# Optimization experiments

Measured on AMD Instinct MI355X. Metric: run time of the kernel, lower is better.

## Reference

```python
import jax, jax.numpy as jnp
import numpy as np

DT = 3600.0  # Euler step size (seconds)
N = 2_097_152  # number of timesteps = len(t)


def _get_AB(params):
    """Build the 3x3 A and 3x5 B RC-network matrices from the 7 parameters."""
    Cai, Cwe, Cwi, Re, Ri, Rw, Rg = (params[i] for i in range(7))
    z = jnp.zeros((), params.dtype)
    A = jnp.stack([
        jnp.stack([-1.0 / Cai * (1.0 / Rg + 1.0 / Ri), z, 1.0 / (Cai * Ri)]),
        jnp.stack([z, -1.0 / Cwe * (1.0 / Re + 1.0 / Rw), 1.0 / (Cwe * Rw)]),
        jnp.stack([1.0 / (Cwi * Ri), 1.0 / (Cwi * Rw), -1.0 / Cwi * (1.0 / Rw + 1.0 / Ri)]),
    ])  # [3,3]
    B = jnp.stack([
        jnp.stack([1.0 / (Cai * Rg), 1.0 / Cai, 1.0 / Cai, z, z]),
        jnp.stack([1.0 / (Cwe * Re), z, z, 1.0 / Cwe, z]),
        jnp.stack([z, z, z, z, 1.0 / Cwi]),
    ])  # [3,5]
    return A, B


def setup_inputs() -> dict:
    key = jax.random.key(0)
    d = jax.random.normal(key, (N, 5), dtype=jnp.float32)  # disturbance inputs per step
    params = jnp.array([100000.0, 30000.0, 300000.0, 10.0, 1.0, 10.0, 10.0], dtype=jnp.float32)
    x0 = jnp.array([20.0, 30.0, 26.0], dtype=jnp.float32)  # initial state temps
    return {"params": params, "x0": x0, "d": d}


def reference(params, x0, d):
    # One explicit-Euler step per timestep:
    #   x_{i+1} = x_i + dt*(A x_i + B d_i) = M x_i + c_i,  M = I + dt*A, c_i = dt*B d_i
    A, B = _get_AB(params)
    M = jnp.eye(3, dtype=params.dtype) + DT * A  # [3,3]
    c = DT * (d[:-1] @ B.T)  # [N-1,3]; last row of d is unused (loop runs len(t)-1 steps)

    def step(x, ci):
        xn = M @ x + ci
        return xn, xn

    _, xs = jax.lax.scan(step, x0, c)  # xs: [N-1,3]
    return jnp.concatenate([x0[None, :], xs], axis=0)  # [N,3] == x_all
```

## Files before the change

kernel.cpp:

```cpp
#include <hip/hip_runtime.h>


static constexpr long STEPS = 2097151;
static constexpr int  SEG   = 8;
static constexpr int  TPB   = 256;
static constexpr int  NBLK  = 1024;
static constexpr long NSEGT = (long)NBLK*TPB;

struct Coef {
    float m00,m02,m11,m12,m20,m21,m22;
    float b00,b01,b10,b13,b24;
};

__device__ __forceinline__ Coef derive(const float* __restrict__ p){
    Coef o;
    const float dt = 3600.0f;
    float Cai=p[0],Cwe=p[1],Cwi=p[2],Re=p[3],Ri=p[4],Rw=p[5],Rg=p[6];
    o.m00 = 1.0f + dt * (-1.0f/Cai*(1.0f/Rg + 1.0f/Ri));
    o.m02 = dt * (1.0f/(Cai*Ri));
    o.m11 = 1.0f + dt * (-1.0f/Cwe*(1.0f/Re + 1.0f/Rw));
    o.m12 = dt * (1.0f/(Cwe*Rw));
    o.m20 = dt * (1.0f/(Cwi*Ri));
    o.m21 = dt * (1.0f/(Cwi*Rw));
    o.m22 = 1.0f + dt * (-1.0f/Cwi*(1.0f/Rw + 1.0f/Ri));
    o.b00 = dt * (1.0f/(Cai*Rg));
    o.b01 = dt * (1.0f/Cai);
    o.b10 = dt * (1.0f/(Cwe*Re));
    o.b13 = dt * (1.0f/Cwe);
    o.b24 = dt * (1.0f/Cwi);
    return o;
}

__device__ __forceinline__ void step(const Coef& C, float& s0, float& s1, float& s2,
                                     float d0, float d1, float d2, float d3, float d4){
    float c0 = fmaf(C.b00, d0, C.b01*(d1+d2));
    float c1 = fmaf(C.b10, d0, C.b13*d3);
    float c2 = C.b24*d4;
    float n0 = fmaf(C.m00, s0, fmaf(C.m02, s2, c0));
    float n1 = fmaf(C.m11, s1, fmaf(C.m12, s2, c1));
    float n2 = fmaf(C.m20, s0, fmaf(C.m21, s1, fmaf(C.m22, s2, c2)));
    s0=n0; s1=n1; s2=n2;
}

__device__ __forceinline__ void mm3(const double* X, const double* Y, double* Z){
    #pragma unroll
    for (int r=0;r<3;++r)
        #pragma unroll
        for (int c=0;c<3;++c)
            Z[r*3+c] = X[r*3+0]*Y[0*3+c] + X[r*3+1]*Y[1*3+c] + X[r*3+2]*Y[2*3+c];
}
__device__ __forceinline__ void msq(double* X){ double T[9]; mm3(X,X,T);
    #pragma unroll
    for (int i=0;i<9;++i) X[i]=T[i]; }

__device__ __forceinline__ void computeM(const float* __restrict__ p, double* Md){
    double Cai=p[0],Cwe=p[1],Cwi=p[2],Re=p[3],Ri=p[4],Rw=p[5],Rg=p[6];
    const double dt = 3600.0;
    Md[0]=1.0 - dt*((1.0/Rg + 1.0/Ri)/Cai); Md[1]=0.0;                              Md[2]=dt/(Cai*Ri);
    Md[3]=0.0;                              Md[4]=1.0 - dt*((1.0/Re + 1.0/Rw)/Cwe); Md[5]=dt/(Cwe*Rw);
    Md[6]=dt/(Cwi*Ri);                      Md[7]=dt/(Cwi*Rw);                      Md[8]=1.0 - dt*((1.0/Rw + 1.0/Ri)/Cwi);
}

__device__ __forceinline__ void seg_sum(const float* __restrict__ d, long i0, const Coef& C,
                                        float& s0, float& s1, float& s2){
    const float4* dp = (const float4*)(d + i0*5);
    s0=0.f; s1=0.f; s2=0.f;
    #pragma unroll
    for (int g=0; g<2; ++g){
        float4 q0=dp[g*5+0], q1=dp[g*5+1], q2=dp[g*5+2], q3=dp[g*5+3], q4=dp[g*5+4];
        step(C,s0,s1,s2, q0.x,q0.y,q0.z,q0.w,q1.x);
        step(C,s0,s1,s2, q1.y,q1.z,q1.w,q2.x,q2.y);
        step(C,s0,s1,s2, q2.z,q2.w,q3.x,q3.y,q3.z);
        step(C,s0,s1,s2, q3.w,q4.x,q4.y,q4.z,q4.w);
    }
}

__global__ __launch_bounds__(256) void k_tot(const float* __restrict__ d,
                                             const float* __restrict__ p,
                                             float* __restrict__ blkTot){
    int t = threadIdx.x, b = blockIdx.x;
    long k = (long)b*TPB + t;
    Coef C = derive(p);
    float s0,s1,s2;
    seg_sum(d, k*SEG, C, s0,s1,s2);

    __shared__ float a[TPB*3];
    a[t*3+0]=s0; a[t*3+1]=s1; a[t*3+2]=s2;
    double Qd[9]; computeM(p, Qd);
    msq(Qd); msq(Qd); msq(Qd);
    __syncthreads();
    for (int off=1; off<TPB; off<<=1){
        float Qf[9];
        #pragma unroll
        for (int i=0;i<9;++i) Qf[i]=(float)Qd[i];
        if ((t & (2*off-1))==0){
            float l0=a[t*3+0], l1=a[t*3+1], l2=a[t*3+2];
            float r0=a[(t+off)*3+0], r1=a[(t+off)*3+1], r2=a[(t+off)*3+2];
            a[t*3+0] = r0 + Qf[0]*l0+Qf[1]*l1+Qf[2]*l2;
            a[t*3+1] = r1 + Qf[3]*l0+Qf[4]*l1+Qf[5]*l2;
            a[t*3+2] = r2 + Qf[6]*l0+Qf[7]*l1+Qf[8]*l2;
        }
        msq(Qd);
        __syncthreads();
    }
    if (t==0){ blkTot[b*3+0]=a[0]; blkTot[b*3+1]=a[1]; blkTot[b*3+2]=a[2]; }
}

__global__ __launch_bounds__(256) void k_scan(const float* __restrict__ d,
                                              const float* __restrict__ p,
                                              const float* __restrict__ blkTot,
                                              const float* __restrict__ x0,
                                              float* __restrict__ out){
    __shared__ float Tl[NBLK*3];
    __shared__ float Wl[TPB*3];
    __shared__ float Sl[TPB*3];
    __shared__ float powA[8][9];
    __shared__ float powB[8][9];
    __shared__ float Rm[9];

    int t = threadIdx.x, b = blockIdx.x;
    long k = (long)b*TPB + t;
    long i0 = k*SEG;
    Coef C = derive(p);

    for (int i=t; i<NBLK*3; i+=TPB) Tl[i] = blkTot[i];

    if (t==0){
        double Qd[9]; computeM(p, Qd);
        msq(Qd); msq(Qd); msq(Qd);
        for (int l=0;l<8;++l){
            #pragma unroll
            for (int i=0;i<9;++i) powA[l][i]=(float)Qd[i];
            msq(Qd);
        }
        #pragma unroll
        for (int i=0;i<9;++i) Rm[i]=(float)Qd[i];
        msq(Qd); msq(Qd);
        for (int l=0;l<8;++l){
            #pragma unroll
            for (int i=0;i<9;++i) powB[l][i]=(float)Qd[i];
            msq(Qd);
        }
    }
    __syncthreads();

    float x00=x0[0], x01=x0[1], x02=x0[2];
    if (t==0){
        Tl[0] += Rm[0]*x00+Rm[1]*x01+Rm[2]*x02;
        Tl[1] += Rm[3]*x00+Rm[4]*x01+Rm[5]*x02;
        Tl[2] += Rm[6]*x00+Rm[7]*x01+Rm[8]*x02;
    }
    __syncthreads();

    float w0=Tl[(4*t)*3+0], w1=Tl[(4*t)*3+1], w2=Tl[(4*t)*3+2];
    #pragma unroll
    for (int j=1;j<4;++j){
        float n0 = Tl[(4*t+j)*3+0] + Rm[0]*w0+Rm[1]*w1+Rm[2]*w2;
        float n1 = Tl[(4*t+j)*3+1] + Rm[3]*w0+Rm[4]*w1+Rm[5]*w2;
        float n2 = Tl[(4*t+j)*3+2] + Rm[6]*w0+Rm[7]*w1+Rm[8]*w2;
        w0=n0; w1=n1; w2=n2;
    }
    Wl[t*3+0]=w0; Wl[t*3+1]=w1; Wl[t*3+2]=w2;
    __syncthreads();
    for (int l=0;l<8;++l){
        int off = 1<<l;
        float y0=0.f,y1=0.f,y2=0.f;
        if (t>=off){ y0=Wl[(t-off)*3+0]; y1=Wl[(t-off)*3+1]; y2=Wl[(t-off)*3+2]; }
        __syncthreads();
        if (t>=off){
            w0 += powB[l][0]*y0+powB[l][1]*y1+powB[l][2]*y2;
            w1 += powB[l][3]*y0+powB[l][4]*y1+powB[l][5]*y2;
            w2 += powB[l][6]*y0+powB[l][7]*y1+powB[l][8]*y2;
            Wl[t*3+0]=w0; Wl[t*3+1]=w1; Wl[t*3+2]=w2;
        }
        __syncthreads();
    }

    float c0,c1,c2;
    if (b==0){ c0=x00; c1=x01; c2=x02; }
    else {
        int e = b-1, q = e>>2;
        float P0=0.f,P1=0.f,P2=0.f;
        if (q>0){ P0=Wl[(q-1)*3+0]; P1=Wl[(q-1)*3+1]; P2=Wl[(q-1)*3+2]; }
        for (int j=4*q; j<=e; ++j){
            float n0 = Tl[j*3+0] + Rm[0]*P0+Rm[1]*P1+Rm[2]*P2;
            float n1 = Tl[j*3+1] + Rm[3]*P0+Rm[4]*P1+Rm[5]*P2;
            float n2 = Tl[j*3+2] + Rm[6]*P0+Rm[7]*P1+Rm[8]*P2;
            P0=n0; P1=n1; P2=n2;
        }
        c0=P0; c1=P1; c2=P2;
    }

    float s0,s1,s2;
    seg_sum(d, i0, C, s0,s1,s2);
    float v0=s0, v1=s1, v2=s2;
    if (t==0){
        v0 += powA[0][0]*c0+powA[0][1]*c1+powA[0][2]*c2;
        v1 += powA[0][3]*c0+powA[0][4]*c1+powA[0][5]*c2;
        v2 += powA[0][6]*c0+powA[0][7]*c1+powA[0][8]*c2;
    }
    Sl[t*3+0]=v0; Sl[t*3+1]=v1; Sl[t*3+2]=v2;
    __syncthreads();
    for (int l=0;l<8;++l){
        int off = 1<<l;
        float y0=0.f,y1=0.f,y2=0.f;
        if (t>=off){ y0=Sl[(t-off)*3+0]; y1=Sl[(t-off)*3+1]; y2=Sl[(t-off)*3+2]; }
        __syncthreads();
        if (t>=off){
            v0 += powA[l][0]*y0+powA[l][1]*y1+powA[l][2]*y2;
            v1 += powA[l][3]*y0+powA[l][4]*y1+powA[l][5]*y2;
            v2 += powA[l][6]*y0+powA[l][7]*y1+powA[l][8]*y2;
            Sl[t*3+0]=v0; Sl[t*3+1]=v1; Sl[t*3+2]=v2;
        }
        __syncthreads();
    }

    float g0,g1,g2;
    if (t==0){ g0=c0; g1=c1; g2=c2; }
    else     { g0=Sl[(t-1)*3+0]; g1=Sl[(t-1)*3+1]; g2=Sl[(t-1)*3+2]; }

    if (k==0){ out[0]=x00; out[1]=x01; out[2]=x02; }
    const float4* dp = (const float4*)(d + i0*5);
    float* op = out + (i0+1)*3;
    bool full = (k != NSEGT-1);
    #pragma unroll
    for (int g=0; g<2; ++g){
        float4 q0=dp[g*5+0], q1=dp[g*5+1], q2=dp[g*5+2], q3=dp[g*5+3], q4=dp[g*5+4];
        step(C,g0,g1,g2, q0.x,q0.y,q0.z,q0.w,q1.x);
        op[(g*4+0)*3+0]=g0; op[(g*4+0)*3+1]=g1; op[(g*4+0)*3+2]=g2;
        step(C,g0,g1,g2, q1.y,q1.z,q1.w,q2.x,q2.y);
        op[(g*4+1)*3+0]=g0; op[(g*4+1)*3+1]=g1; op[(g*4+1)*3+2]=g2;
        step(C,g0,g1,g2, q2.z,q2.w,q3.x,q3.y,q3.z);
        op[(g*4+2)*3+0]=g0; op[(g*4+2)*3+1]=g1; op[(g*4+2)*3+2]=g2;
        step(C,g0,g1,g2, q3.w,q4.x,q4.y,q4.z,q4.w);
        if (g==1 && !full) break;
        op[(g*4+3)*3+0]=g0; op[(g*4+3)*3+1]=g1; op[(g*4+3)*3+2]=g2;
    }
}

extern "C" void kernel_launch(void* const* d_in, const int* in_sizes, int n_in,
                              void* d_out, int out_size, void* d_ws, size_t ws_size,
                              hipStream_t stream) {
    const float* params = (const float*)d_in[0];
    const float* x0     = (const float*)d_in[1];
    const float* d      = (const float*)d_in[2];
    float* out    = (float*)d_out;
    float* blkTot = (float*)d_ws;

    k_tot <<<NBLK, TPB, 0, stream>>>(d, params, blkTot);
    k_scan<<<NBLK, TPB, 0, stream>>>(d, params, blkTot, x0, out);
}
```

Baseline: 45.84 us.

## Stage chunk inputs through LDS with coalesced loads and stores, restructure block-carry scan

Both kernels now load each block's 2048-row chunk of d into shared memory with fully coalesced float4 reads, replacing strided per-thread float4 reads. k_tot uses a strided intra-thread recurrence, binary matrix-power weighting and wavefront shuffle reductions in place of a shared-memory tree. A new extra block precomputes matrix power tables into the workspace. k_scan computes each block's carry directly from all block totals with power tables and stages outputs in LDS for coalesced float4 stores. This adds shared-memory use (about 40KB per block) and redundant carry work per block, which may reduce occupancy and depends on the extra block finishing before k_scan reads the tables.

Result: slower. 48.85 us (+6.6%).

```diff
diff --git a/kernel.cpp b/kernel.cpp
--- a/kernel.cpp
+++ b/kernel.cpp
@@ -1,11 +1,13 @@
 #include <hip/hip_runtime.h>
 
 
-static constexpr long STEPS = 2097151;
-static constexpr int  SEG   = 8;
 static constexpr int  TPB   = 256;
+static constexpr int  CHUNK = 2048;
 static constexpr int  NBLK  = 1024;
-static constexpr long NSEGT = (long)NBLK*TPB;
+static constexpr long NROW  = 2097152;
+
+#define WS_TOT 0
+#define WS_TAB 3072
 
 struct Coef {
     float m00,m02,m11,m12,m20,m21,m22;
@@ -61,180 +63,239 @@
     Md[6]=dt/(Cwi*Ri);                      Md[7]=dt/(Cwi*Rw);                      Md[8]=1.0 - dt*((1.0/Rw + 1.0/Ri)/Cwi);
 }
 
-__device__ __forceinline__ void seg_sum(const float* __restrict__ d, long i0, const Coef& C,
-                                        float& s0, float& s1, float& s2){
-    const float4* dp = (const float4*)(d + i0*5);
-    s0=0.f; s1=0.f; s2=0.f;
-    #pragma unroll
-    for (int g=0; g<2; ++g){
-        float4 q0=dp[g*5+0], q1=dp[g*5+1], q2=dp[g*5+2], q3=dp[g*5+3], q4=dp[g*5+4];
-        step(C,s0,s1,s2, q0.x,q0.y,q0.z,q0.w,q1.x);
-        step(C,s0,s1,s2, q1.y,q1.z,q1.w,q2.x,q2.y);
-        step(C,s0,s1,s2, q2.z,q2.w,q3.x,q3.y,q3.z);
-        step(C,s0,s1,s2, q3.w,q4.x,q4.y,q4.z,q4.w);
-    }
-}
-
 __global__ __launch_bounds__(256) void k_tot(const float* __restrict__ d,
                                              const float* __restrict__ p,
-                                             float* __restrict__ blkTot){
+                                             float* __restrict__ ws){
     int t = threadIdx.x, b = blockIdx.x;
-    long k = (long)b*TPB + t;
+    if (b == NBLK){
+        if (t == 0){
+            double A[9], M0[9], T[9];
+            computeM(p, M0);
+            #pragma unroll
+            for (int i=0;i<9;++i) A[i]=M0[i];
+            for (int k=1;k<=8;++k){
+                for (int i=0;i<9;++i) ws[WS_TAB + (k-1)*9 + i] = (float)A[i];
+                if (k<8){ mm3(M0, A, T); for(int i=0;i<9;++i) A[i]=T[i]; }
+            }
+            for (int l=0;l<8;++l){
+                for (int i=0;i<9;++i) ws[WS_TAB + 72 + l*9 + i] = (float)A[i];
+                msq(A);
+            }
+            for (int i2=0;i2<10;++i2){
+                for (int i=0;i<9;++i) ws[WS_TAB + 144 + i2*9 + i] = (float)A[i];
+                msq(A);
+            }
+        }
+        return;
+    }
+
+    __shared__ float sh[CHUNK*5];
+    __shared__ float Pw[8][9];
+    __shared__ float Gg[9];
+    __shared__ float wred[4][3];
+
+    long base = (long)b * CHUNK;
+    const float4* gsrc = (const float4*)(d + base*5);
+    float4* sh4 = (float4*)sh;
+    float4 stg[10];
+    #pragma unroll
+    for (int g=0; g<10; ++g) stg[g] = gsrc[g*TPB + t];
+    if (t == 0){
+        double A[9]; computeM(p, A);
+        for (int i2=0;i2<8;++i2){
+            for (int i=0;i<9;++i) Pw[i2][i] = (float)A[i];
+            msq(A);
+        }
+        for (int i=0;i<9;++i) Gg[i] = (float)A[i];
+    }
+    #pragma unroll
+    for (int g=0; g<10; ++g) sh4[g*TPB + t] = stg[g];
+    __syncthreads();
+
     Coef C = derive(p);
-    float s0,s1,s2;
-    seg_sum(d, k*SEG, C, s0,s1,s2);
-
-    __shared__ float a[TPB*3];
-    a[t*3+0]=s0; a[t*3+1]=s1; a[t*3+2]=s2;
-    double Qd[9]; computeM(p, Qd);
-    msq(Qd); msq(Qd); msq(Qd);
-    __syncthreads();
-    for (int off=1; off<TPB; off<<=1){
-        float Qf[9];
-        #pragma unroll
-        for (int i=0;i<9;++i) Qf[i]=(float)Qd[i];
-        if ((t & (2*off-1))==0){
-            float l0=a[t*3+0], l1=a[t*3+1], l2=a[t*3+2];
-            float r0=a[(t+off)*3+0], r1=a[(t+off)*3+1], r2=a[(t+off)*3+2];
-            a[t*3+0] = r0 + Qf[0]*l0+Qf[1]*l1+Qf[2]*l2;
-            a[t*3+1] = r1 + Qf[3]*l0+Qf[4]*l1+Qf[5]*l2;
-            a[t*3+2] = r2 + Qf[6]*l0+Qf[7]*l1+Qf[8]*l2;
-        }
-        msq(Qd);
-        __syncthreads();
-    }
-    if (t==0){ blkTot[b*3+0]=a[0]; blkTot[b*3+1]=a[1]; blkTot[b*3+2]=a[2]; }
+    float v0,v1,v2;
+    {
+        const float* r = &sh[t*5];
+        v0 = fmaf(C.b00, r[0], C.b01*(r[1]+r[2]));
+        v1 = fmaf(C.b10, r[0], C.b13*r[3]);
+        v2 = C.b24*r[4];
+    }
+    #pragma unroll
+    for (int j=1;j<8;++j){
+        const float* r = &sh[(j*TPB + t)*5];
+        float c0 = fmaf(C.b00, r[0], C.b01*(r[1]+r[2]));
+        float c1 = fmaf(C.b10, r[0], C.b13*r[3]);
+        float c2 = C.b24*r[4];
+        float n0 = Gg[0]*v0+Gg[1]*v1+Gg[2]*v2 + c0;
+        float n1 = Gg[3]*v0+Gg[4]*v1+Gg[5]*v2 + c1;
+        float n2 = Gg[6]*v0+Gg[7]*v1+Gg[8]*v2 + c2;
+        v0=n0;v1=n1;v2=n2;
+    }
+    int e = 255 - t;
+    #pragma unroll
+    for (int i2=0;i2<8;++i2){
+        float m0 = Pw[i2][0]*v0+Pw[i2][1]*v1+Pw[i2][2]*v2;
+        float m1 = Pw[i2][3]*v0+Pw[i2][4]*v1+Pw[i2][5]*v2;
+        float m2 = Pw[i2][6]*v0+Pw[i2][7]*v1+Pw[i2][8]*v2;
+        bool bit = (e>>i2)&1;
+        v0 = bit?m0:v0; v1 = bit?m1:v1; v2 = bit?m2:v2;
+    }
+    #pragma unroll
+    for (int m=1;m<64;m<<=1){
+        v0 += __shfl_xor(v0, m, 64);
+        v1 += __shfl_xor(v1, m, 64);
+        v2 += __shfl_xor(v2, m, 64);
+    }
+    int wv = t>>6, ln = t&63;
+    if (ln==0){ wred[wv][0]=v0; wred[wv][1]=v1; wred[wv][2]=v2; }
+    __syncthreads();
+    if (t==0){
+        ws[WS_TOT + b*3+0] = wred[0][0]+wred[1][0]+wred[2][0]+wred[3][0];
+        ws[WS_TOT + b*3+1] = wred[0][1]+wred[1][1]+wred[2][1]+wred[3][1];
+        ws[WS_TOT + b*3+2] = wred[0][2]+wred[1][2]+wred[2][2]+wred[3][2];
+    }
 }
 
 __global__ __launch_bounds__(256) void k_scan(const float* __restrict__ d,
                                               const float* __restrict__ p,
-                                              const float* __restrict__ blkTot,
+                                              const float* __restrict__ ws,
                                               const float* __restrict__ x0,
                                               float* __restrict__ out){
-    __shared__ float Tl[NBLK*3];
-    __shared__ float Wl[TPB*3];
-    __shared__ float Sl[TPB*3];
-    __shared__ float powA[8][9];
-    __shared__ float powB[8][9];
-    __shared__ float Rm[9];
+    __shared__ float BUF[CHUNK*5];
+    __shared__ float tab[234];
+    __shared__ float wred[4][3];
+    __shared__ float carryL[3];
 
     int t = threadIdx.x, b = blockIdx.x;
-    long k = (long)b*TPB + t;
-    long i0 = k*SEG;
+    long base = (long)b * CHUNK;
+    const float4* gsrc = (const float4*)(d + base*5);
+    float4* sh4 = (float4*)BUF;
+    float4 stg[10];
+    #pragma unroll
+    for (int g=0; g<10; ++g) stg[g] = gsrc[g*TPB + t];
+    if (t < 234) tab[t] = ws[WS_TAB + t];
+    #pragma unroll
+    for (int g=0; g<10; ++g) sh4[g*TPB + t] = stg[g];
+    __syncthreads();
+
     Coef C = derive(p);
-
-    for (int i=t; i<NBLK*3; i+=TPB) Tl[i] = blkTot[i];
-
+    float px[8][3];
+    {
+        float s0=0.f, s1=0.f, s2=0.f;
+        #pragma unroll
+        for (int j=0;j<8;++j){
+            const float* r = &BUF[(8*t + j)*5];
+            step(C, s0,s1,s2, r[0],r[1],r[2],r[3],r[4]);
+            px[j][0]=s0; px[j][1]=s1; px[j][2]=s2;
+        }
+    }
+
+    float w0=0.f, w1=0.f, w2=0.f;
+    if (t < b){
+        int e = b-1-t;
+        int m = e>>8, u = e&255;
+        const float* G2 = &tab[144 + 8*9];
+        float a0 = ws[WS_TOT + t*3+0], a1 = ws[WS_TOT + t*3+1], a2 = ws[WS_TOT + t*3+2];
+        for (int j=1;j<=m;++j){
+            int kk = 256*j + t;
+            float n0 = G2[0]*a0+G2[1]*a1+G2[2]*a2 + ws[WS_TOT+kk*3+0];
+            float n1 = G2[3]*a0+G2[4]*a1+G2[5]*a2 + ws[WS_TOT+kk*3+1];
+            float n2 = G2[6]*a0+G2[7]*a1+G2[8]*a2 + ws[WS_TOT+kk*3+2];
+            a0=n0;a1=n1;a2=n2;
+        }
+        #pragma unroll
+        for (int i2=0;i2<8;++i2){
+            const float* P = &tab[144 + i2*9];
+            float m0 = P[0]*a0+P[1]*a1+P[2]*a2;
+            float m1 = P[3]*a0+P[4]*a1+P[5]*a2;
+            float m2 = P[6]*a0+P[7]*a1+P[8]*a2;
+            bool bit = (u>>i2)&1;
+            a0 = bit?m0:a0; a1=bit?m1:a1; a2=bit?m2:a2;
+        }
+        w0=a0; w1=a1; w2=a2;
+    }
+    if (t == 0){
+        float a0=x0[0], a1=x0[1], a2=x0[2];
+        #pragma unroll
+        for (int i2=0;i2<10;++i2){
+            const float* P = &tab[144 + i2*9];
+            float m0 = P[0]*a0+P[1]*a1+P[2]*a2;
+            float m1 = P[3]*a0+P[4]*a1+P[5]*a2;
+            float m2 = P[6]*a0+P[7]*a1+P[8]*a2;
+            bool bit = (b>>i2)&1;
+            a0 = bit?m0:a0; a1=bit?m1:a1; a2=bit?m2:a2;
+        }
+        w0+=a0; w1+=a1; w2+=a2;
+    }
+    #pragma unroll
+    for (int m2v=1;m2v<64;m2v<<=1){
+        w0 += __shfl_xor(w0, m2v, 64);
+        w1 += __shfl_xor(w1, m2v, 64);
+        w2 += __shfl_xor(w2, m2v, 64);
+    }
+    int wv=t>>6, ln=t&63;
+    if (ln==0){ wred[wv][0]=w0; wred[wv][1]=w1; wred[wv][2]=w2; }
+    __syncthreads();
     if (t==0){
-        double Qd[9]; computeM(p, Qd);
-        msq(Qd); msq(Qd); msq(Qd);
-        for (int l=0;l<8;++l){
-            #pragma unroll
-            for (int i=0;i<9;++i) powA[l][i]=(float)Qd[i];
-            msq(Qd);
-        }
-        #pragma unroll
-        for (int i=0;i<9;++i) Rm[i]=(float)Qd[i];
-        msq(Qd); msq(Qd);
-        for (int l=0;l<8;++l){
-            #pragma unroll
-            for (int i=0;i<9;++i) powB[l][i]=(float)Qd[i];
-            msq(Qd);
-        }
-    }
-    __syncthreads();
-
-    float x00=x0[0], x01=x0[1], x02=x0[2];
+        carryL[0]=wred[0][0]+wred[1][0]+wred[2][0]+wred[3][0];
+        carryL[1]=wred[0][1]+wred[1][1]+wred[2][1]+wred[3][1];
+        carryL[2]=wred[0][2]+wred[1][2]+wred[2][2]+wred[3][2];
+    }
+    __syncthreads();
+    float c0=carryL[0], c1=carryL[1], c2=carryL[2];
+
+    float* Sl = &BUF[8192];
+    float z0=px[7][0], z1=px[7][1], z2=px[7][2];
     if (t==0){
-        Tl[0] += Rm[0]*x00+Rm[1]*x01+Rm[2]*x02;
-        Tl[1] += Rm[3]*x00+Rm[4]*x01+Rm[5]*x02;
-        Tl[2] += Rm[6]*x00+Rm[7]*x01+Rm[8]*x02;
-    }
-    __syncthreads();
-
-    float w0=Tl[(4*t)*3+0], w1=Tl[(4*t)*3+1], w2=Tl[(4*t)*3+2];
-    #pragma unroll
-    for (int j=1;j<4;++j){
-        float n0 = Tl[(4*t+j)*3+0] + Rm[0]*w0+Rm[1]*w1+Rm[2]*w2;
-        float n1 = Tl[(4*t+j)*3+1] + Rm[3]*w0+Rm[4]*w1+Rm[5]*w2;
-        float n2 = Tl[(4*t+j)*3+2] + Rm[6]*w0+Rm[7]*w1+Rm[8]*w2;
-        w0=n0; w1=n1; w2=n2;
-    }
-    Wl[t*3+0]=w0; Wl[t*3+1]=w1; Wl[t*3+2]=w2;
-    __syncthreads();
+        const float* M8 = &tab[72];
+        z0 += M8[0]*c0+M8[1]*c1+M8[2]*c2;
+        z1 += M8[3]*c0+M8[4]*c1+M8[5]*c2;
+        z2 += M8[6]*c0+M8[7]*c1+M8[8]*c2;
+    }
+    Sl[t*3+0]=z0; Sl[t*3+1]=z1; Sl[t*3+2]=z2;
+    __syncthreads();
+    #pragma unroll
     for (int l=0;l<8;++l){
-        int off = 1<<l;
-        float y0=0.f,y1=0.f,y2=0.f;
-        if (t>=off){ y0=Wl[(t-off)*3+0]; y1=Wl[(t-off)*3+1]; y2=Wl[(t-off)*3+2]; }
-        __syncthreads();
-        if (t>=off){
-            w0 += powB[l][0]*y0+powB[l][1]*y1+powB[l][2]*y2;
-            w1 += powB[l][3]*y0+powB[l][4]*y1+powB[l][5]*y2;
-            w2 += powB[l][6]*y0+powB[l][7]*y1+powB[l][8]*y2;
-            Wl[t*3+0]=w0; Wl[t*3+1]=w1; Wl[t*3+2]=w2;
-        }
-        __syncthreads();
-    }
-
-    float c0,c1,c2;
-    if (b==0){ c0=x00; c1=x01; c2=x02; }
-    else {
-        int e = b-1, q = e>>2;
-        float P0=0.f,P1=0.f,P2=0.f;
-        if (q>0){ P0=Wl[(q-1)*3+0]; P1=Wl[(q-1)*3+1]; P2=Wl[(q-1)*3+2]; }
-        for (int j=4*q; j<=e; ++j){
-            float n0 = Tl[j*3+0] + Rm[0]*P0+Rm[1]*P1+Rm[2]*P2;
-            float n1 = Tl[j*3+1] + Rm[3]*P0+Rm[4]*P1+Rm[5]*P2;
-            float n2 = Tl[j*3+2] + Rm[6]*P0+Rm[7]*P1+Rm[8]*P2;
-            P0=n0; P1=n1; P2=n2;
-        }
-        c0=P0; c1=P1; c2=P2;
-    }
-
-    float s0,s1,s2;
-    seg_sum(d, i0, C, s0,s1,s2);
-    float v0=s0, v1=s1, v2=s2;
-    if (t==0){
-        v0 += powA[0][0]*c0+powA[0][1]*c1+powA[0][2]*c2;
-        v1 += powA[0][3]*c0+powA[0][4]*c1+powA[0][5]*c2;
-        v2 += powA[0][6]*c0+powA[0][7]*c1+powA[0][8]*c2;
-    }
-    Sl[t*3+0]=v0; Sl[t*3+1]=v1; Sl[t*3+2]=v2;
-    __syncthreads();
-    for (int l=0;l<8;++l){
+        const float* P = &tab[72 + l*9];
         int off = 1<<l;
         float y0=0.f,y1=0.f,y2=0.f;
         if (t>=off){ y0=Sl[(t-off)*3+0]; y1=Sl[(t-off)*3+1]; y2=Sl[(t-off)*3+2]; }
         __syncthreads();
         if (t>=off){
-            v0 += powA[l][0]*y0+powA[l][1]*y1+powA[l][2]*y2;
-            v1 += powA[l][3]*y0+powA[l][4]*y1+powA[l][5]*y2;
-            v2 += powA[l][6]*y0+powA[l][7]*y1+powA[l][8]*y2;
-            Sl[t*3+0]=v0; Sl[t*3+1]=v1; Sl[t*3+2]=v2;
+            z0 += P[0]*y0+P[1]*y1+P[2]*y2;
+            z1 += P[3]*y0+P[4]*y1+P[5]*y2;
+            z2 += P[6]*y0+P[7]*y1+P[8]*y2;
+            Sl[t*3+0]=z0; Sl[t*3+1]=z1; Sl[t*3+2]=z2;
         }
         __syncthreads();
     }
-
-    float g0,g1,g2;
-    if (t==0){ g0=c0; g1=c1; g2=c2; }
-    else     { g0=Sl[(t-1)*3+0]; g1=Sl[(t-1)*3+1]; g2=Sl[(t-1)*3+2]; }
-
-    if (k==0){ out[0]=x00; out[1]=x01; out[2]=x02; }
-    const float4* dp = (const float4*)(d + i0*5);
-    float* op = out + (i0+1)*3;
-    bool full = (k != NSEGT-1);
-    #pragma unroll
-    for (int g=0; g<2; ++g){
-        float4 q0=dp[g*5+0], q1=dp[g*5+1], q2=dp[g*5+2], q3=dp[g*5+3], q4=dp[g*5+4];
-        step(C,g0,g1,g2, q0.x,q0.y,q0.z,q0.w,q1.x);
-        op[(g*4+0)*3+0]=g0; op[(g*4+0)*3+1]=g1; op[(g*4+0)*3+2]=g2;
-        step(C,g0,g1,g2, q1.y,q1.z,q1.w,q2.x,q2.y);
-        op[(g*4+1)*3+0]=g0; op[(g*4+1)*3+1]=g1; op[(g*4+1)*3+2]=g2;
-        step(C,g0,g1,g2, q2.z,q2.w,q3.x,q3.y,q3.z);
-        op[(g*4+2)*3+0]=g0; op[(g*4+2)*3+1]=g1; op[(g*4+2)*3+2]=g2;
-        step(C,g0,g1,g2, q3.w,q4.x,q4.y,q4.z,q4.w);
-        if (g==1 && !full) break;
-        op[(g*4+3)*3+0]=g0; op[(g*4+3)*3+1]=g1; op[(g*4+3)*3+2]=g2;
+    float s0,s1,s2;
+    if (t==0){ s0=c0; s1=c1; s2=c2; }
+    else     { s0=Sl[(t-1)*3+0]; s1=Sl[(t-1)*3+1]; s2=Sl[(t-1)*3+2]; }
+
+    float* ost = BUF;
+    #pragma unroll
+    for (int j=0;j<8;++j){
+        const float* P = &tab[j*9];
+        float o0 = px[j][0] + P[0]*s0+P[1]*s1+P[2]*s2;
+        float o1 = px[j][1] + P[3]*s0+P[4]*s1+P[5]*s2;
+        float o2 = px[j][2] + P[6]*s0+P[7]*s1+P[8]*s2;
+        int q = 24*t + 3 + 3*j;
+        ost[q+0]=o0; ost[q+1]=o1; ost[q+2]=o2;
+    }
+    __syncthreads();
+    float* og = out + base*3;
+    const float4* ost4 = (const float4*)ost;
+    float4* og4 = (float4*)og;
+    #pragma unroll
+    for (int g=0; g<6; ++g){
+        int f = g*TPB + t;
+        if (f != 0) og4[f] = ost4[f];
+    }
+    if (t == 0){
+        og[3] = ost[3];
+        if (b == 0){ out[0]=x0[0]; out[1]=x0[1]; out[2]=x0[2]; }
+        if (b != NBLK-1){ og[6144]=ost[6144]; og[6145]=ost[6145]; og[6146]=ost[6146]; }
     }
 }
 
@@ -244,9 +305,9 @@
     const float* params = (const float*)d_in[0];
     const float* x0     = (const float*)d_in[1];
     const float* d      = (const float*)d_in[2];
-    float* out    = (float*)d_out;
-    float* blkTot = (float*)d_ws;
-
-    k_tot <<<NBLK, TPB, 0, stream>>>(d, params, blkTot);
-    k_scan<<<NBLK, TPB, 0, stream>>>(d, params, blkTot, x0, out);
-}
+    float* out = (float*)d_out;
+    float* ws  = (float*)d_ws;
+
+    k_tot <<<NBLK+1, TPB, 0, stream>>>(d, params, ws);
+    k_scan<<<NBLK,   TPB, 0, stream>>>(d, params, ws, x0, out);
+}
```
